# Optimization experiments

Hardware: AMD Instinct MI355X
Metric: run time of the kernel (lower is better)

The kernel has to match this reference:

```python
import jax, jax.numpy as jnp
import numpy as np

D = 768


def _rope(x):
    # interleaved RoPE over the FULL hidden dim (applied before head split, as in source)
    S, d = x.shape[-2], x.shape[-1]
    pos = jnp.arange(S, dtype=x.dtype)[:, None]                      # [S,1]
    theta = jnp.power(jnp.asarray(10000.0, x.dtype),
                      -2.0 * jnp.arange(d // 2, dtype=x.dtype) / d)  # [d/2]
    ang = pos * theta                                                # [S,d/2]
    cos2 = jnp.repeat(jnp.cos(ang), 2, axis=-1)                      # [S,d]
    sin2 = jnp.repeat(jnp.sin(ang), 2, axis=-1)
    x2 = jnp.stack([-x[..., 1::2], x[..., ::2]], axis=-1).reshape(x.shape)
    return x * cos2 + x2 * sin2


def _attn(q_in, kv_in, wq, bq, wk, bk, wv, bv, n_heads):
    # shared core of SelfAttention (n_heads=1) and MultiheadAttention (n_heads=8)
    B, Sq, Dm = q_in.shape
    Sk = kv_in.shape[1]
    Q = _rope(q_in @ wq + bq)
    K = _rope(kv_in @ wk + bk)
    V = kv_in @ wv + bv
    hd = Dm // n_heads
    Q = Q.reshape(B, Sq, n_heads, hd).transpose(0, 2, 1, 3)
    K = K.reshape(B, Sk, n_heads, hd).transpose(0, 2, 1, 3)
    V = V.reshape(B, Sk, n_heads, hd).transpose(0, 2, 1, 3)
    scores = jnp.einsum('bhqd,bhkd->bhqk', Q, K) * 8.0  # source multiplies by 8, no 1/sqrt(d)
    p = jax.nn.softmax(scores, axis=-1)
    out = jnp.einsum('bhqk,bhkd->bhqd', p, V)
    return out.transpose(0, 2, 1, 3).reshape(B, Sq, Dm)


def _ffn(x, w1, b1, w2, b2):
    return jax.nn.silu(x @ w1 + b1) @ w2 + b2


def _gate(x):
    # F = F * softmax(F, -1) + F
    return x * jax.nn.softmax(x, axis=-1) + x


def setup_inputs() -> dict:
    key = jax.random.key(0)
    ks = jax.random.split(key, 32)
    B, S, L = 32, 512, 100
    s = 1.0 / np.sqrt(D)

    def lin(k):
        kw, kb = jax.random.split(k)
        return (jax.random.normal(kw, (D, D), jnp.float32) * s,
                jax.random.normal(kb, (D,), jnp.float32) * 0.01)

    inp = {}
    inp['text_embedding'] = jax.random.normal(ks[0], (B, S, D), jnp.float32)
    inp['visual_ids'] = jax.random.randint(ks[1], (B, S), 0, L)
    inp['acoustic_ids'] = jax.random.randint(ks[2], (B, S), 0, L)
    # embedding tables (label_size+1 rows, last row is padding_idx -> zeros)
    vt = jax.random.normal(ks[3], (L + 1, D), jnp.float32)
    at = jax.random.normal(ks[4], (L + 1, D), jnp.float32)
    inp['vis_table'] = vt.at[L].set(0.0)
    inp['ac_table'] = at.at[L].set(0.0)
    (inp['hv_wq'], inp['hv_bq']) = lin(ks[5])
    (inp['hv_wk'], inp['hv_bk']) = lin(ks[6])
    (inp['hv_wv'], inp['hv_bv']) = lin(ks[7])
    (inp['ha_wq'], inp['ha_bq']) = lin(ks[8])
    (inp['ha_wk'], inp['ha_bk']) = lin(ks[9])
    (inp['ha_wv'], inp['ha_bv']) = lin(ks[10])
    (inp['ht_wq'], inp['ht_bq']) = lin(ks[11])
    (inp['ht_wk'], inp['ht_bk']) = lin(ks[12])
    (inp['ht_wv'], inp['ht_bv']) = lin(ks[13])
    (inp['ht_fcw'], inp['ht_fcb']) = lin(ks[14])
    (inp['ffn_w1'], inp['ffn_b1']) = lin(ks[15])
    (inp['ffn_w2'], inp['ffn_b2']) = lin(ks[16])
    kw, kb = jax.random.split(ks[17])
    inp['cat_w'] = jax.random.normal(kw, (2 * D, D), jnp.float32) * (1.0 / np.sqrt(2 * D))
    inp['cat_b'] = jax.random.normal(kb, (D,), jnp.float32) * 0.01
    return inp


def reference(text_embedding, vis_table, ac_table,
              hv_wq, hv_bq, hv_wk, hv_bk, hv_wv, hv_bv,
              ha_wq, ha_bq, ha_wk, ha_bk, ha_wv, ha_bv,
              ht_wq, ht_bq, ht_wk, ht_bk, ht_wv, ht_bv, ht_fcw, ht_fcb,
              ffn_w1, ffn_b1, ffn_w2, ffn_b2, cat_w, cat_b,
              visual_ids, acoustic_ids):
    hv = lambda q, kv: _attn(q, kv, hv_wq, hv_bq, hv_wk, hv_bk, hv_wv, hv_bv, 1)
    ha = lambda q, kv: _attn(q, kv, ha_wq, ha_bq, ha_wk, ha_bk, ha_wv, ha_bv, 1)

    visual_ = vis_table[visual_ids]       # [B,S,D]
    acoustic_ = ac_table[acoustic_ids]

    visual_ = hv(text_embedding, visual_)
    acoustic_ = ha(text_embedding, acoustic_)

    F1 = jnp.concatenate([visual_, acoustic_], axis=-1) @ cat_w + cat_b
    F1 = _ffn(_gate(F1), ffn_w1, ffn_b1, ffn_w2, ffn_b2)

    v = hv(visual_, acoustic_)
    a = ha(acoustic_, visual_)
    F2 = jnp.concatenate([v, a], axis=-1) @ cat_w + cat_b
    F2 = _ffn(_gate(F2), ffn_w1, ffn_b1, ffn_w2, ffn_b2)

    F3 = _attn(F1, text_embedding, ht_wq, ht_bq, ht_wk, ht_bk, ht_wv, ht_bv, 8)
    F3 = F3 @ ht_fcw + ht_fcb
    F3 = _ffn(_gate(F3), ffn_w1, ffn_b1, ffn_w2, ffn_b2)

    es = text_embedding + F1 + F2 + F3
    return _gate(es)
```

## Files before the change

kernel.cpp:

```cpp
#include <hip/hip_runtime.h>
#include <stdint.h>
#include <math.h>


typedef unsigned short USH;
typedef __attribute__((ext_vector_type(8))) short short8;
typedef __attribute__((ext_vector_type(4))) float floatx4;

#define MFMA16(a, b, c) __builtin_amdgcn_mfma_f32_16x16x32_bf16((a), (b), (c), 0, 0, 0)

static constexpr int NB = 32;
static constexpr int SS = 512;
static constexpr int DD = 768;
static constexpr int MM = NB * SS;

__device__ __forceinline__ float bf2f(USH h) {
    return __uint_as_float(((unsigned)h) << 16);
}
__device__ __forceinline__ USH f2bf(float x) {
    unsigned u = __float_as_uint(x);
    return (USH)((u + 0x7fffu + ((u >> 16) & 1u)) >> 16);
}
__device__ __forceinline__ void split3(float x, USH &h, USH &m, USH &l) {
    h = f2bf(x);
    const float r1 = x - bf2f(h);
    m = f2bf(r1);
    const float r2 = r1 - bf2f(m);
    l = f2bf(r2);
}
__device__ __forceinline__ void split3x8(const float* v, short8 &H, short8 &M, short8 &L) {
#pragma unroll
    for (int j = 0; j < 8; ++j) {
        USH h, m, l;
        split3(v[j], h, m, l);
        H[j] = (short)h; M[j] = (short)m; L[j] = (short)l;
    }
}
__device__ __forceinline__ uint2 pk4(USH a, USH b, USH c, USH d) {
    uint2 r;
    r.x = (unsigned)a | ((unsigned)b << 16);
    r.y = (unsigned)c | ((unsigned)d << 16);
    return r;
}

struct TransArgs {
    const float* in[13];
    USH* o0[13]; USH* o1[13]; USH* o2[13];
    int R[13];
};

__global__ __launch_bounds__(256) void trans_k(TransArgs a) {
    const int mi = blockIdx.z;
    const float* __restrict__ in = a.in[mi];
    USH* __restrict__ o0 = a.o0[mi];
    USH* __restrict__ o1 = a.o1[mi];
    USH* __restrict__ o2 = a.o2[mi];
    const int R = a.R[mi];
    const int bx = blockIdx.x, by = blockIdx.y;
    if (bx * 32 >= R) return;
    __shared__ float t[32][33];
    const int tx = threadIdx.x & 31, ty = threadIdx.x >> 5;
#pragma unroll
    for (int i = 0; i < 4; ++i)
        t[ty + i * 8][tx] = in[(size_t)(bx * 32 + ty + i * 8) * 768 + by * 32 + tx];
    __syncthreads();
#pragma unroll
    for (int i = 0; i < 4; ++i) {
        USH h, m, l;
        split3(t[tx][ty + i * 8], h, m, l);
        const size_t o = (size_t)(by * 32 + ty + i * 8) * R + bx * 32 + tx;
        o0[o] = h; o1[o] = m; o2[o] = l;
    }
}

__global__ __launch_bounds__(256) void gather_k(const int* __restrict__ ids,
                                                const float* __restrict__ table,
                                                float* __restrict__ dst) {
    const int g  = blockIdx.x * 256 + threadIdx.x;
    const int m  = g / 192;
    const int c4 = (g - m * 192) * 4;
    const int id = ids[m];
    *(float4*)(dst + (size_t)m * DD + c4) =
        *(const float4*)(table + (size_t)id * DD + c4);
}

__global__ __launch_bounds__(256) void gemm_k(
    const float* __restrict__ A0, const float* __restrict__ A1,
    const USH* __restrict__ B0, const USH* __restrict__ B1, const USH* __restrict__ B2,
    int ldb, const float* __restrict__ bias,
    float* __restrict__ C, USH* __restrict__ S0p, USH* __restrict__ S1p,
    USH* __restrict__ S2p, int K, int act, int tout, int Mc)
{
    __shared__ __align__(16) USH sA0[4096], sA1[4096], sA2[4096];
    __shared__ __align__(16) USH sB0[4096], sB1[4096], sB2[4096];

    const int tid  = threadIdx.x;
    const int lane = tid & 63;
    const int w    = tid >> 6;
    const int quad = lane >> 4, l15 = lane & 15;
    const int wm = (w >> 1) * 64, wn = (w & 1) * 64;
    const int gm0 = blockIdx.x * 128, gn0 = blockIdx.y * 128;

    const int i0 = tid * 2, i1 = tid * 2 + 1;
    const int r0 = i0 >> 2, c0 = (i0 & 3) << 3;
    const int r1 = i1 >> 2, c1 = (i1 & 3) << 3;

    const floatx4 zero = {0.f, 0.f, 0.f, 0.f};
    floatx4 acc[4][4];
#pragma unroll
    for (int i = 0; i < 4; ++i)
#pragma unroll
        for (int j = 0; j < 4; ++j) acc[i][j] = zero;

    for (int k0 = 0; k0 < K; k0 += 32) {
        const float* __restrict__ A = (k0 < 768) ? A0 : A1;
        const int kof = (k0 < 768) ? k0 : (k0 - 768);

        *(uint4*)&sB0[r0 * 32 + c0] = *(const uint4*)(B0 + (size_t)(gn0 + r0) * ldb + k0 + c0);
        *(uint4*)&sB0[r1 * 32 + c1] = *(const uint4*)(B0 + (size_t)(gn0 + r1) * ldb + k0 + c1);
        *(uint4*)&sB1[r0 * 32 + c0] = *(const uint4*)(B1 + (size_t)(gn0 + r0) * ldb + k0 + c0);
        *(uint4*)&sB1[r1 * 32 + c1] = *(const uint4*)(B1 + (size_t)(gn0 + r1) * ldb + k0 + c1);
        *(uint4*)&sB2[r0 * 32 + c0] = *(const uint4*)(B2 + (size_t)(gn0 + r0) * ldb + k0 + c0);
        *(uint4*)&sB2[r1 * 32 + c1] = *(const uint4*)(B2 + (size_t)(gn0 + r1) * ldb + k0 + c1);

#pragma unroll
        for (int u = 0; u < 4; ++u) {
            const int idx = tid + u * 256;
            const int r = idx >> 3, c = (idx & 7) * 4;
            const float4 v = *(const float4*)(A + (size_t)(gm0 + r) * 768 + kof + c);
            USH h[4], m[4], l[4];
            split3(v.x, h[0], m[0], l[0]);
            split3(v.y, h[1], m[1], l[1]);
            split3(v.z, h[2], m[2], l[2]);
            split3(v.w, h[3], m[3], l[3]);
            *(uint2*)&sA0[r * 32 + c] = pk4(h[0], h[1], h[2], h[3]);
            *(uint2*)&sA1[r * 32 + c] = pk4(m[0], m[1], m[2], m[3]);
            *(uint2*)&sA2[r * 32 + c] = pk4(l[0], l[1], l[2], l[3]);
        }
        __syncthreads();

        short8 a0[4], a1f[4], a2[4], b0[4], b1f[4], b2[4];
#pragma unroll
        for (int t = 0; t < 4; ++t) {
            const int ao = (wm + t * 16 + l15) * 32 + quad * 8;
            const int bo = (wn + t * 16 + l15) * 32 + quad * 8;
            a0[t]  = *(const short8*)&sA0[ao];
            a1f[t] = *(const short8*)&sA1[ao];
            a2[t]  = *(const short8*)&sA2[ao];
            b0[t]  = *(const short8*)&sB0[bo];
            b1f[t] = *(const short8*)&sB1[bo];
            b2[t]  = *(const short8*)&sB2[bo];
        }
#pragma unroll
        for (int i = 0; i < 4; ++i)
#pragma unroll
            for (int j = 0; j < 4; ++j) acc[i][j] = MFMA16(a0[i],  b0[j],  acc[i][j]);
#pragma unroll
        for (int i = 0; i < 4; ++i)
#pragma unroll
            for (int j = 0; j < 4; ++j) acc[i][j] = MFMA16(a0[i],  b1f[j], acc[i][j]);
#pragma unroll
        for (int i = 0; i < 4; ++i)
#pragma unroll
            for (int j = 0; j < 4; ++j) acc[i][j] = MFMA16(a1f[i], b0[j],  acc[i][j]);
#pragma unroll
        for (int i = 0; i < 4; ++i)
#pragma unroll
            for (int j = 0; j < 4; ++j) acc[i][j] = MFMA16(a0[i],  b2[j],  acc[i][j]);
#pragma unroll
        for (int i = 0; i < 4; ++i)
#pragma unroll
            for (int j = 0; j < 4; ++j) acc[i][j] = MFMA16(a2[i],  b0[j],  acc[i][j]);
#pragma unroll
        for (int i = 0; i < 4; ++i)
#pragma unroll
            for (int j = 0; j < 4; ++j) acc[i][j] = MFMA16(a1f[i], b1f[j], acc[i][j]);
        __syncthreads();
    }

#pragma unroll
    for (int j = 0; j < 4; ++j) {
        const int col = gn0 + wn + j * 16 + l15;
        const float bv = bias[col];
#pragma unroll
        for (int i = 0; i < 4; ++i) {
#pragma unroll
            for (int r = 0; r < 4; ++r) {
                const int row = gm0 + wm + i * 16 + quad * 4 + r;
                float x = acc[i][j][r] + bv;
                if (act == 1) {
                    const float s = 1.0f / (1.0f + expf(-x));
                    x = x * s;
                }
                if (tout == 1) {
                    USH hh, mm2, ll;
                    split3(x, hh, mm2, ll);
                    const size_t o = (size_t)col * Mc + row;
                    S0p[o] = hh; S1p[o] = mm2; S2p[o] = ll;
                } else if (tout == 2) {
                    C[(size_t)col * Mc + row] = x;
                } else {
                    C[(size_t)row * 768 + col] = x;
                }
            }
        }
    }
}

__global__ __launch_bounds__(256) void tab_k(float* __restrict__ tab) {
    const int p = blockIdx.x * 256 + threadIdx.x;
    const int s = p / 384;
    const int i = p - s * 384;
    const float ef = (-2.0f * (float)i) / 768.0f;
    const float th = (float)pow(10000.0, (double)ef);
    const float ang = (float)s * th;
    float sn, cs;
    sincosf(ang, &sn, &cs);
    tab[2 * p]     = cs;
    tab[2 * p + 1] = sn;
}

__global__ __launch_bounds__(256) void rope_k(float* __restrict__ X) {
    const int p = blockIdx.x * 256 + threadIdx.x;
    const int m = p / 384;
    const int i = p - m * 384;
    const int s = m & (SS - 1);
    const float ef = (-2.0f * (float)i) / 768.0f;
    const float th = (float)pow(10000.0, (double)ef);
    const float ang = (float)s * th;
    float sn, cs;
    sincosf(ang, &sn, &cs);
    float2 x = *(float2*)(X + (size_t)m * DD + 2 * i);
    float2 y;
    y.x = x.x * cs - x.y * sn;
    y.y = x.y * cs + x.x * sn;
    *(float2*)(X + (size_t)m * DD + 2 * i) = y;
}

__global__ __launch_bounds__(256) void rope_tab_k(float* __restrict__ X,
                                                  const float* __restrict__ tab) {
    const int p = blockIdx.x * 256 + threadIdx.x;
    const int m = p / 384;
    const int i = p - m * 384;
    const int s = m & (SS - 1);
    const float2 t = *(const float2*)(tab + 2 * (s * 384 + i));
    float2 x = *(float2*)(X + (size_t)m * DD + 2 * i);
    float2 y;
    y.x = x.x * t.x - x.y * t.y;
    y.y = x.y * t.x + x.x * t.y;
    *(float2*)(X + (size_t)m * DD + 2 * i) = y;
}

__global__ __launch_bounds__(256) void rope_split_tab_k(
    const float* __restrict__ X, const float* __restrict__ tab,
    USH* __restrict__ P0, USH* __restrict__ P1, USH* __restrict__ P2)
{
    const int p = blockIdx.x * 256 + threadIdx.x;
    const int m = p / 384;
    const int i = p - m * 384;
    const int s = m & (SS - 1);
    const float2 t = *(const float2*)(tab + 2 * (s * 384 + i));
    const float2 x = *(const float2*)(X + (size_t)m * DD + 2 * i);
    float2 y;
    y.x = x.x * t.x - x.y * t.y;
    y.y = x.y * t.x + x.x * t.y;
    USH h0, m0, l0, h1, m1, l1;
    split3(y.x, h0, m0, l0);
    split3(y.y, h1, m1, l1);
    const size_t o = (size_t)m * DD + 2 * i;
    *(unsigned*)&P0[o] = (unsigned)h0 | ((unsigned)h1 << 16);
    *(unsigned*)&P1[o] = (unsigned)m0 | ((unsigned)m1 << 16);
    *(unsigned*)&P2[o] = (unsigned)l0 | ((unsigned)l1 << 16);
}

__global__ __launch_bounds__(256) void attn_fast_k(
    const float* __restrict__ Q,
    const USH* __restrict__ KH, const USH* __restrict__ KM, const USH* __restrict__ KL,
    const USH* __restrict__ VH, const USH* __restrict__ VM, const USH* __restrict__ VL,
    float* __restrict__ O, int H, int hd, int Mc)
{
    __shared__ __align__(16) float S[16][520];
    __shared__ __align__(16) USH P2buf[16 * 520];
    __shared__ float red[16][16];
    __shared__ float stat[16];

    const int tid  = threadIdx.x;
    const int lane = tid & 63;
    const int w    = tid >> 6;
    const int quad = lane >> 4, l15 = lane & 15;
    const int b = blockIdx.y / H;
    const int h = blockIdx.y - b * H;
    const int q0 = blockIdx.x * 16;

    const floatx4 zero = {0.f, 0.f, 0.f, 0.f};

    floatx4 acc[8];
#pragma unroll
    for (int t = 0; t < 8; ++t) acc[t] = zero;

    const size_t qbase  = ((size_t)(b * SS + q0 + l15)) * DD + h * hd;
    const size_t kstrip = ((size_t)(b * SS + w * 128 + l15)) * DD + h * hd;
    const int nks = hd >> 5;
    for (int ks = 0; ks < nks; ++ks) {
        const int co = ks * 32 + quad * 8;
        float qv[8];
        *(float4*)&qv[0] = *(const float4*)(Q + qbase + co);
        *(float4*)&qv[4] = *(const float4*)(Q + qbase + co + 4);
        short8 qh, qm, ql;
        split3x8(qv, qh, qm, ql);

        size_t ka = kstrip + co;
        short8 khc = *(const short8*)&KH[ka];
        short8 kmc = *(const short8*)&KM[ka];
        short8 klc = *(const short8*)&KL[ka];
#pragma unroll
        for (int t = 0; t < 8; ++t) {
            short8 khn = khc, kmn = kmc, kln = klc;
            if (t < 7) {
                const size_t kb = ka + (size_t)(t + 1) * 16 * DD;
                khn = *(const short8*)&KH[kb];
                kmn = *(const short8*)&KM[kb];
                kln = *(const short8*)&KL[kb];
            }
            acc[t] = MFMA16(qh, khc, acc[t]);
            acc[t] = MFMA16(qh, kmc, acc[t]);
            acc[t] = MFMA16(qm, khc, acc[t]);
            acc[t] = MFMA16(qh, klc, acc[t]);
            acc[t] = MFMA16(ql, khc, acc[t]);
            acc[t] = MFMA16(qm, kmc, acc[t]);
            __builtin_amdgcn_sched_barrier(0);
            khc = khn; kmc = kmn; klc = kln;
        }
    }
#pragma unroll
    for (int t = 0; t < 8; ++t)
#pragma unroll
        for (int r = 0; r < 4; ++r)
            S[quad * 4 + r][w * 128 + t * 16 + l15] = acc[t][r] * 8.0f;
    __syncthreads();

    const int row = tid >> 4, c16 = tid & 15;
    const int cb = c16 * 32;
    float mx = -3.4e38f;
#pragma unroll 8
    for (int c = 0; c < 32; ++c) mx = fmaxf(mx, S[row][cb + c]);
    red[row][c16] = mx;
    __syncthreads();
    if (c16 == 0) {
        float m2 = red[row][0];
#pragma unroll
        for (int j = 1; j < 16; ++j) m2 = fmaxf(m2, red[row][j]);
        stat[row] = m2;
    }
    __syncthreads();
    mx = stat[row];
    float ev[32];
    float sum = 0.f;
#pragma unroll 8
    for (int c = 0; c < 32; ++c) {
        ev[c] = expf(S[row][cb + c] - mx);
        sum += ev[c];
    }
    red[row][c16] = sum;
    __syncthreads();
    if (c16 == 0) {
        float s2 = 0.f;
#pragma unroll
        for (int j = 0; j < 16; ++j) s2 += red[row][j];
        stat[row] = s2;
    }
    __syncthreads();
    const float den = stat[row];
    USH* const P0 = (USH*)&S[0][0];
    USH* const P1 = P0 + 16 * 520;
    USH* const P2 = P2buf;
#pragma unroll 8
    for (int c = 0; c < 32; ++c) {
        const float pr = ev[c] / den;
        USH hh, mm, ll;
        split3(pr, hh, mm, ll);
        P0[row * 520 + cb + c] = hh;
        P1[row * 520 + cb + c] = mm;
        P2[row * 520 + cb + c] = ll;
    }
    __syncthreads();

    const int nnt = hd >> 4;
    for (int nt = w; nt < nnt; nt += 4) {
        floatx4 o = zero;
        const int colg = h * hd + nt * 16 + l15;
        const size_t vb = (size_t)colg * Mc + b * SS;
#pragma unroll 2
        for (int ks = 0; ks < 16; ++ks) {
            const int ko = ks * 32 + quad * 8;
            const short8 ph = *(const short8*)&P0[l15 * 520 + ko];
            const short8 pm = *(const short8*)&P1[l15 * 520 + ko];
            const short8 pl = *(const short8*)&P2[l15 * 520 + ko];
            const short8 vh = *(const short8*)&VH[vb + ko];
            const short8 vm = *(const short8*)&VM[vb + ko];
            const short8 vl = *(const short8*)&VL[vb + ko];
            o = MFMA16(ph, vh, o);
            o = MFMA16(ph, vm, o);
            o = MFMA16(pm, vh, o);
            o = MFMA16(ph, vl, o);
            o = MFMA16(pl, vh, o);
            o = MFMA16(pm, vm, o);
        }
#pragma unroll
        for (int r = 0; r < 4; ++r) {
            const int orow = b * SS + q0 + quad * 4 + r;
            O[(size_t)orow * 768 + colg] = o[r];
        }
    }
}

__global__ __launch_bounds__(256) void attn_k(
    const float* __restrict__ Q, const float* __restrict__ Kp,
    const float* __restrict__ Vt, float* __restrict__ O,
    int H, int hd, int Mc)
{
    __shared__ __align__(16) float S[16][520];
    __shared__ __align__(16) USH P2buf[16 * 520];
    __shared__ float red[16][16];
    __shared__ float stat[16];

    const int tid  = threadIdx.x;
    const int lane = tid & 63;
    const int w    = tid >> 6;
    const int quad = lane >> 4, l15 = lane & 15;
    const int b = blockIdx.y / H;
    const int h = blockIdx.y - b * H;
    const int q0 = blockIdx.x * 16;

    const floatx4 zero = {0.f, 0.f, 0.f, 0.f};

    floatx4 acc[8];
#pragma unroll
    for (int t = 0; t < 8; ++t) acc[t] = zero;

    const size_t qbase = ((size_t)(b * SS + q0 + l15)) * DD + h * hd;
    const int nks = hd >> 5;
    for (int ks = 0; ks < nks; ++ks) {
        const int co = ks * 32 + quad * 8;
        float qv[8];
        *(float4*)&qv[0] = *(const float4*)(Q + qbase + co);
        *(float4*)&qv[4] = *(const float4*)(Q + qbase + co + 4);
        short8 qh, qm, ql;
        split3x8(qv, qh, qm, ql);
#pragma unroll
        for (int t = 0; t < 8; ++t) {
            const size_t kb = ((size_t)(b * SS + w * 128 + t * 16 + l15)) * DD + h * hd + co;
            float kv[8];
            *(float4*)&kv[0] = *(const float4*)(Kp + kb);
            *(float4*)&kv[4] = *(const float4*)(Kp + kb + 4);
            short8 kh, km, kl;
            split3x8(kv, kh, km, kl);
            acc[t] = MFMA16(qh, kh, acc[t]);
            acc[t] = MFMA16(qh, km, acc[t]);
            acc[t] = MFMA16(qm, kh, acc[t]);
            acc[t] = MFMA16(qh, kl, acc[t]);
            acc[t] = MFMA16(ql, kh, acc[t]);
            acc[t] = MFMA16(qm, km, acc[t]);
        }
    }
#pragma unroll
    for (int t = 0; t < 8; ++t)
#pragma unroll
        for (int r = 0; r < 4; ++r)
            S[quad * 4 + r][w * 128 + t * 16 + l15] = acc[t][r] * 8.0f;
    __syncthreads();

    const int row = tid >> 4, c16 = tid & 15;
    const int cb = c16 * 32;
    float mx = -3.4e38f;
#pragma unroll 8
    for (int c = 0; c < 32; ++c) mx = fmaxf(mx, S[row][cb + c]);
    red[row][c16] = mx;
    __syncthreads();
    if (c16 == 0) {
        float m2 = red[row][0];
#pragma unroll
        for (int j = 1; j < 16; ++j) m2 = fmaxf(m2, red[row][j]);
        stat[row] = m2;
    }
    __syncthreads();
    mx = stat[row];
    float ev[32];
    float sum = 0.f;
#pragma unroll 8
    for (int c = 0; c < 32; ++c) {
        ev[c] = expf(S[row][cb + c] - mx);
        sum += ev[c];
    }
    red[row][c16] = sum;
    __syncthreads();
    if (c16 == 0) {
        float s2 = 0.f;
#pragma unroll
        for (int j = 0; j < 16; ++j) s2 += red[row][j];
        stat[row] = s2;
    }
    __syncthreads();
    const float den = stat[row];
    USH* const P0 = (USH*)&S[0][0];
    USH* const P1 = P0 + 16 * 520;
    USH* const P2 = P2buf;
#pragma unroll 8
    for (int c = 0; c < 32; ++c) {
        const float pr = ev[c] / den;
        USH hh, mm, ll;
        split3(pr, hh, mm, ll);
        P0[row * 520 + cb + c] = hh;
        P1[row * 520 + cb + c] = mm;
        P2[row * 520 + cb + c] = ll;
    }
    __syncthreads();

    const int nnt = hd >> 4;
    for (int nt = w; nt < nnt; nt += 4) {
        floatx4 o = zero;
        const int colg = h * hd + nt * 16 + l15;
        const size_t vb = (size_t)colg * Mc + b * SS;
        for (int ks = 0; ks < 16; ++ks) {
            const int ko = ks * 32 + quad * 8;
            const short8 ph = *(const short8*)&P0[l15 * 520 + ko];
            const short8 pm = *(const short8*)&P1[l15 * 520 + ko];
            const short8 pl = *(const short8*)&P2[l15 * 520 + ko];
            float vv[8];
            *(float4*)&vv[0] = *(const float4*)(Vt + vb + ko);
            *(float4*)&vv[4] = *(const float4*)(Vt + vb + ko + 4);
            short8 vh, vm, vl;
            split3x8(vv, vh, vm, vl);
            o = MFMA16(ph, vh, o);
            o = MFMA16(ph, vm, o);
            o = MFMA16(pm, vh, o);
            o = MFMA16(ph, vl, o);
            o = MFMA16(pl, vh, o);
            o = MFMA16(pm, vm, o);
        }
#pragma unroll
        for (int r = 0; r < 4; ++r) {
            const int orow = b * SS + q0 + quad * 4 + r;
            O[(size_t)orow * 768 + colg] = o[r];
        }
    }
}

__global__ __launch_bounds__(256) void gate_k(float* __restrict__ X) {
    __shared__ float red[256];
    const int r = blockIdx.x, tid = threadIdx.x;
    const size_t base = (size_t)r * DD;
    float x[3];
#pragma unroll
    for (int j = 0; j < 3; ++j) x[j] = X[base + tid + j * 256];
    float mx = fmaxf(x[0], fmaxf(x[1], x[2]));
    red[tid] = mx;
    __syncthreads();
    for (int s = 128; s > 0; s >>= 1) {
        if (tid < s) red[tid] = fmaxf(red[tid], red[tid + s]);
        __syncthreads();
    }
    mx = red[0];
    __syncthreads();
    float e[3];
    float sum = 0.f;
#pragma unroll
    for (int j = 0; j < 3; ++j) { e[j] = expf(x[j] - mx); sum += e[j]; }
    red[tid] = sum;
    __syncthreads();
    for (int s = 128; s > 0; s >>= 1) {
        if (tid < s) red[tid] += red[tid + s];
        __syncthreads();
    }
    const float den = red[0];
#pragma unroll
    for (int j = 0; j < 3; ++j)
        X[base + tid + j * 256] = x[j] * (e[j] / den) + x[j];
}

__global__ __launch_bounds__(256) void final_k(
    const float* __restrict__ text,
    const float* __restrict__ F1, const float* __restrict__ F2,
    const float* __restrict__ F3, float* __restrict__ out)
{
    __shared__ float red[256];
    const int r = blockIdx.x, tid = threadIdx.x;
    const size_t base = (size_t)r * DD;
    float x[3];
#pragma unroll
    for (int j = 0; j < 3; ++j) {
        const int c = tid + j * 256;
        x[j] = ((text[base + c] + F1[base + c]) + F2[base + c]) + F3[base + c];
    }
    float mx = fmaxf(x[0], fmaxf(x[1], x[2]));
    red[tid] = mx;
    __syncthreads();
    for (int s = 128; s > 0; s >>= 1) {
        if (tid < s) red[tid] = fmaxf(red[tid], red[tid + s]);
        __syncthreads();
    }
    mx = red[0];
    __syncthreads();
    float e[3];
    float sum = 0.f;
#pragma unroll
    for (int j = 0; j < 3; ++j) { e[j] = expf(x[j] - mx); sum += e[j]; }
    red[tid] = sum;
    __syncthreads();
    for (int s = 128; s > 0; s >>= 1) {
        if (tid < s) red[tid] += red[tid + s];
        __syncthreads();
    }
    const float den = red[0];
#pragma unroll
    for (int j = 0; j < 3; ++j) {
        const int c = tid + j * 256;
        out[base + c] = x[j] * (e[j] / den) + x[j];
    }
}

extern "C" void kernel_launch(void* const* d_in, const int* in_sizes, int n_in,
                              void* d_out, int out_size, void* d_ws, size_t ws_size,
                              hipStream_t stream)
{
    (void)in_sizes; (void)n_in; (void)out_size;

    const float* text    = (const float*)d_in[0];
    const int*   vis_ids = (const int*)d_in[1];
    const int*   ac_ids  = (const int*)d_in[2];
    const float* vis_tab = (const float*)d_in[3];
    const float* ac_tab  = (const float*)d_in[4];
    const float* hv_wq = (const float*)d_in[5],  *hv_bq = (const float*)d_in[6];
    const float* hv_wk = (const float*)d_in[7],  *hv_bk = (const float*)d_in[8];
    const float* hv_wv = (const float*)d_in[9],  *hv_bv = (const float*)d_in[10];
    const float* ha_wq = (const float*)d_in[11], *ha_bq = (const float*)d_in[12];
    const float* ha_wk = (const float*)d_in[13], *ha_bk = (const float*)d_in[14];
    const float* ha_wv = (const float*)d_in[15], *ha_bv = (const float*)d_in[16];
    const float* ht_wq = (const float*)d_in[17], *ht_bq = (const float*)d_in[18];
    const float* ht_wk = (const float*)d_in[19], *ht_bk = (const float*)d_in[20];
    const float* ht_wv = (const float*)d_in[21], *ht_bv = (const float*)d_in[22];
    const float* ht_fcw = (const float*)d_in[23], *ht_fcb = (const float*)d_in[24];
    const float* ffn_w1 = (const float*)d_in[25], *ffn_b1 = (const float*)d_in[26];
    const float* ffn_w2 = (const float*)d_in[27], *ffn_b2 = (const float*)d_in[28];
    const float* cat_w  = (const float*)d_in[29], *cat_b  = (const float*)d_in[30];

    const size_t SQ   = (size_t)768 * 768;
    const size_t WUSH = 3 * (12 * SQ + (size_t)768 * 1536);
    const size_t TABF = (size_t)512 * 384 * 2;
    int Mc = 0, fast = 0;
    for (int cand = MM; cand >= 512; cand >>= 1) {
        const size_t nf = WUSH * sizeof(USH) + TABF * 4 + (size_t)cand * 768 * 28;
        const size_t ns = WUSH * sizeof(USH) + (size_t)cand * 768 * 24;
        if (nf <= ws_size) { Mc = cand; fast = 1; break; }
        if (ns <= ws_size) { Mc = cand; fast = 0; break; }
    }
    if (Mc == 0) return;
    const int nchunk = MM / Mc;
    const int chB    = Mc / SS;

    USH* p = (USH*)d_ws;
    USH *wt0[13], *wt1[13], *wt2[13];
    for (int i = 0; i < 13; ++i) {
        const size_t sz = (i == 12) ? (size_t)768 * 1536 : SQ;
        wt0[i] = p; p += sz;
        wt1[i] = p; p += sz;
        wt2[i] = p; p += sz;
    }

    TransArgs ta;
    const float* tin[13] = {hv_wq, hv_wk, hv_wv, ha_wq, ha_wk, ha_wv,
                            ht_wq, ht_wk, ht_wv, ht_fcw, ffn_w1, ffn_w2, cat_w};
    for (int i = 0; i < 13; ++i) {
        ta.in[i] = tin[i]; ta.o0[i] = wt0[i]; ta.o1[i] = wt1[i]; ta.o2[i] = wt2[i];
        ta.R[i] = (i == 12) ? 1536 : 768;
    }
    trans_k<<<dim3(48, 24, 13), 256, 0, stream>>>(ta);

    const size_t PSZ = (size_t)Mc * 768;
    const dim3 gg(Mc / 128, DD / 128), gb(256);
    const int ropeg = Mc * 384 / 256;
    const float* NULF = nullptr;
    USH* const NUSH = nullptr;

    if (fast) {
        float* tab = (float*)p;
        float* fp  = tab + TABF;
        float *A_ = fp + 0 * PSZ, *B_ = fp + 1 * PSZ;
        float *C_ = fp + 2 * PSZ, *F_ = fp + 3 * PSZ;
        USH* KH = (USH*)(fp + 4 * PSZ);
        USH* KM = KH + PSZ;  USH* KL = KM + PSZ;
        USH* VH = KL + PSZ;  USH* VM = VH + PSZ;  USH* VL = VM + PSZ;

        tab_k<<<(512 * 384) / 256, 256, 0, stream>>>(tab);

#define GEMM(A0P, A1P, WI, LDB, BIAS, CP, KK, ACT) \
    gemm_k<<<gg, gb, 0, stream>>>(A0P, A1P, wt0[WI], wt1[WI], wt2[WI], LDB, BIAS, \
                                  CP, NUSH, NUSH, NUSH, KK, ACT, 0, Mc)
#define GEMMV(A0P, WI, BIAS) \
    gemm_k<<<gg, gb, 0, stream>>>(A0P, NULF, wt0[WI], wt1[WI], wt2[WI], 768, BIAS, \
                                  (float*)nullptr, VH, VM, VL, 768, 0, 1, Mc)
#define ROPE(XP)  rope_tab_k<<<ropeg, 256, 0, stream>>>(XP, tab)
#define RSPL(XP)  rope_split_tab_k<<<ropeg, 256, 0, stream>>>(XP, tab, KH, KM, KL)
#define ATTNF(QP, OP, HH, HD) \
    attn_fast_k<<<dim3(SS / 16, chB * (HH)), 256, 0, stream>>>(QP, KH, KM, KL, \
                                                  VH, VM, VL, OP, HH, HD, Mc)
#define GATE(XP) gate_k<<<Mc, 256, 0, stream>>>(XP)

        for (int c = 0; c < nchunk; ++c) {
            const float* tx = text + (size_t)c * PSZ;
            const int* vi = vis_ids + (size_t)c * Mc;
            const int* ai = ac_ids  + (size_t)c * Mc;
            float* outc = (float*)d_out + (size_t)c * PSZ;

            gather_k<<<Mc * 192 / 256, 256, 0, stream>>>(vi, vis_tab, A_);
            gather_k<<<Mc * 192 / 256, 256, 0, stream>>>(ai, ac_tab, B_);

            GEMM(tx, NULF, 0, 768, hv_bq, C_, 768, 0);
            GEMM(A_, NULF, 1, 768, hv_bk, outc, 768, 0);
            GEMMV(A_, 2, hv_bv);
            ROPE(C_); RSPL(outc);
            ATTNF(C_, F_, 1, 768);

            GEMM(tx, NULF, 3, 768, ha_bq, C_, 768, 0);
            GEMM(B_, NULF, 4, 768, ha_bk, outc, 768, 0);
            GEMMV(B_, 5, ha_bv);
            ROPE(C_); RSPL(outc);
            ATTNF(C_, A_, 1, 768);

            GEMM(F_, NULF, 0, 768, hv_bq, C_, 768, 0);
            GEMM(A_, NULF, 1, 768, hv_bk, outc, 768, 0);
            GEMMV(A_, 2, hv_bv);
            ROPE(C_); RSPL(outc);
            ATTNF(C_, C_, 1, 768);

            GEMM(A_, NULF, 3, 768, ha_bq, B_, 768, 0);
            GEMM(F_, NULF, 4, 768, ha_bk, outc, 768, 0);
            GEMMV(F_, 5, ha_bv);
            ROPE(B_); RSPL(outc);
            ATTNF(B_, B_, 1, 768);

            GEMM(F_, A_, 12, 1536, cat_b, outc, 1536, 0);
            GATE(outc);
            GEMM(outc, NULF, 10, 768, ffn_b1, F_, 768, 1);
            GEMM(F_, NULF, 11, 768, ffn_b2, A_, 768, 0);

            GEMM(C_, B_, 12, 1536, cat_b, outc, 1536, 0);
            GATE(outc);
            GEMM(outc, NULF, 10, 768, ffn_b1, F_, 768, 1);
            GEMM(F_, NULF, 11, 768, ffn_b2, C_, 768, 0);

            GEMM(A_, NULF, 6, 768, ht_bq, B_, 768, 0);
            GEMM(tx, NULF, 7, 768, ht_bk, outc, 768, 0);
            GEMMV(tx, 8, ht_bv);
            ROPE(B_); RSPL(outc);
            ATTNF(B_, B_, 8, 96);
            GEMM(B_, NULF, 9, 768, ht_fcb, F_, 768, 0);
            GATE(F_);
            GEMM(F_, NULF, 10, 768, ffn_b1, B_, 768, 1);
            GEMM(B_, NULF, 11, 768, ffn_b2, F_, 768, 0);

            final_k<<<Mc, 256, 0, stream>>>(tx, A_, C_, F_, outc);
        }
#undef GEMM
#undef GEMMV
#undef ROPE
#undef RSPL
#undef ATTNF
#undef GATE
    } else {
        float* fp = (float*)p;
        float *A_ = fp + 0 * PSZ, *B_ = fp + 1 * PSZ, *C_ = fp + 2 * PSZ;
        float *D_ = fp + 3 * PSZ, *E_ = fp + 4 * PSZ, *F_ = fp + 5 * PSZ;

#define GEMM(A0P, A1P, WI, LDB, BIAS, CP, KK, ACT, TOUT) \
    gemm_k<<<gg, gb, 0, stream>>>(A0P, A1P, wt0[WI], wt1[WI], wt2[WI], LDB, BIAS, \
                                  CP, NUSH, NUSH, NUSH, KK, ACT, TOUT, Mc)
#define ROPE(XP) rope_k<<<ropeg, 256, 0, stream>>>(XP)
#define ATTN(QP, KP, VP, OP, HH, HD) \
    attn_k<<<dim3(SS / 16, chB * (HH)), 256, 0, stream>>>(QP, KP, VP, OP, HH, HD, Mc)
#define GATE(XP) gate_k<<<Mc, 256, 0, stream>>>(XP)

        for (int c = 0; c < nchunk; ++c) {
            const float* tx = text + (size_t)c * PSZ;
            const int* vi = vis_ids + (size_t)c * Mc;
            const int* ai = ac_ids  + (size_t)c * Mc;
            float* outc = (float*)d_out + (size_t)c * PSZ;

            gather_k<<<Mc * 192 / 256, 256, 0, stream>>>(vi, vis_tab, A_);
            gather_k<<<Mc * 192 / 256, 256, 0, stream>>>(ai, ac_tab, B_);

            GEMM(tx, NULF, 0, 768, hv_bq, C_, 768, 0, 0);
            GEMM(A_, NULF, 1, 768, hv_bk, D_, 768, 0, 0);
            GEMM(A_, NULF, 2, 768, hv_bv, E_, 768, 0, 2);
            ROPE(C_); ROPE(D_);
            ATTN(C_, D_, E_, F_, 1, 768);

            GEMM(tx, NULF, 3, 768, ha_bq, C_, 768, 0, 0);
            GEMM(B_, NULF, 4, 768, ha_bk, D_, 768, 0, 0);
            GEMM(B_, NULF, 5, 768, ha_bv, E_, 768, 0, 2);
            ROPE(C_); ROPE(D_);
            ATTN(C_, D_, E_, A_, 1, 768);

            GEMM(F_, NULF, 0, 768, hv_bq, C_, 768, 0, 0);
            GEMM(A_, NULF, 1, 768, hv_bk, D_, 768, 0, 0);
            GEMM(A_, NULF, 2, 768, hv_bv, E_, 768, 0, 2);
            ROPE(C_); ROPE(D_);
            ATTN(C_, D_, E_, C_, 1, 768);

            GEMM(A_, NULF, 3, 768, ha_bq, B_, 768, 0, 0);
            GEMM(F_, NULF, 4, 768, ha_bk, D_, 768, 0, 0);
            GEMM(F_, NULF, 5, 768, ha_bv, E_, 768, 0, 2);
            ROPE(B_); ROPE(D_);
            ATTN(B_, D_, E_, B_, 1, 768);

            GEMM(F_, A_, 12, 1536, cat_b, D_, 1536, 0, 0);
            GATE(D_);
            GEMM(D_, NULF, 10, 768, ffn_b1, E_, 768, 1, 0);
            GEMM(E_, NULF, 11, 768, ffn_b2, F_, 768, 0, 0);

            GEMM(C_, B_, 12, 1536, cat_b, A_, 1536, 0, 0);
            GATE(A_);
            GEMM(A_, NULF, 10, 768, ffn_b1, C_, 768, 1, 0);
            GEMM(C_, NULF, 11, 768, ffn_b2, B_, 768, 0, 0);

            GEMM(F_, NULF, 6, 768, ht_bq, C_, 768, 0, 0);
            GEMM(tx, NULF, 7, 768, ht_bk, D_, 768, 0, 0);
            GEMM(tx, NULF, 8, 768, ht_bv, E_, 768, 0, 2);
            ROPE(C_); ROPE(D_);
            ATTN(C_, D_, E_, C_, 8, 96);
            GEMM(C_, NULF, 9, 768, ht_fcb, A_, 768, 0, 0);
            GATE(A_);
            GEMM(A_, NULF, 10, 768, ffn_b1, C_, 768, 1, 0);
            GEMM(C_, NULF, 11, 768, ffn_b2, D_, 768, 0, 0);

            final_k<<<Mc, 256, 0, stream>>>(tx, F_, B_, D_, outc);
        }
#undef GEMM
#undef ROPE
#undef ATTN
#undef GATE
    }
}
```

Measured before the change: 7.340 ms.

## Pre-split GEMM activations into bf16x3 planes and pipeline attention K/V loads

Activations are now split once into three bf16 planes (hi/mid/lo) by dedicated split, gather-split and gate-split kernels. A new LDS-free GEMM kernel with a 128x96 tile reads those planes directly, instead of re-splitting fp32 inputs inside every tiled GEMM. The fast attention kernel now register-prefetches all eight K and V fragments one step ahead and swizzles the block order. This removes repeated per-GEMM conversion work and improves latency hiding, at the cost of extra split launches, more register pressure, and GEMM operands read straight from global memory without shared-memory reuse.

```diff
diff --git a/kernel.cpp b/kernel.cpp
--- a/kernel.cpp
+++ b/kernel.cpp
@@ -73,6 +73,37 @@
     }
 }
 
+__global__ __launch_bounds__(256) void split_k(const float* __restrict__ X,
+        USH* __restrict__ P0, USH* __restrict__ P1, USH* __restrict__ P2) {
+    const size_t g = (size_t)blockIdx.x * 256 + threadIdx.x;
+    float v[8];
+    *(float4*)&v[0] = ((const float4*)X)[2 * g];
+    *(float4*)&v[4] = ((const float4*)X)[2 * g + 1];
+    short8 H8, M8, L8;
+    split3x8(v, H8, M8, L8);
+    ((short8*)P0)[g] = H8;
+    ((short8*)P1)[g] = M8;
+    ((short8*)P2)[g] = L8;
+}
+
+__global__ __launch_bounds__(256) void gather_split_k(const int* __restrict__ ids,
+        const float* __restrict__ table,
+        USH* __restrict__ P0, USH* __restrict__ P1, USH* __restrict__ P2) {
+    const int g = blockIdx.x * 256 + threadIdx.x;
+    const int m = g / 96;
+    const int e = (g - m * 96) * 8;
+    const int id = ids[m];
+    float v[8];
+    *(float4*)&v[0] = *(const float4*)(table + (size_t)id * DD + e);
+    *(float4*)&v[4] = *(const float4*)(table + (size_t)id * DD + e + 4);
+    short8 H8, M8, L8;
+    split3x8(v, H8, M8, L8);
+    const size_t o = (size_t)m * DD + e;
+    *(short8*)&P0[o] = H8;
+    *(short8*)&P1[o] = M8;
+    *(short8*)&P2[o] = L8;
+}
+
 __global__ __launch_bounds__(256) void gather_k(const int* __restrict__ ids,
                                                 const float* __restrict__ table,
                                                 float* __restrict__ dst) {
@@ -84,12 +115,101 @@
         *(const float4*)(table + (size_t)id * DD + c4);
 }
 
+__global__ __launch_bounds__(256) void gemm_ps_k(
+    const USH* __restrict__ AH0, const USH* __restrict__ AM0, const USH* __restrict__ AL0,
+    const USH* __restrict__ AH1, const USH* __restrict__ AM1, const USH* __restrict__ AL1,
+    const USH* __restrict__ B0, const USH* __restrict__ B1, const USH* __restrict__ B2,
+    int ldb, const float* __restrict__ bias,
+    float* __restrict__ C, USH* __restrict__ S0p, USH* __restrict__ S1p,
+    USH* __restrict__ S2p, int K, int act, int tout, int Mc)
+{
+    const int tid  = threadIdx.x;
+    const int lane = tid & 63;
+    const int w    = tid >> 6;
+    const int quad = lane >> 4, l15 = lane & 15;
+    const int wm = (w >> 1) * 64, wn = (w & 1) * 48;
+    const int gm0 = blockIdx.x * 128, gn0 = blockIdx.y * 96;
+
+    const floatx4 zero = {0.f, 0.f, 0.f, 0.f};
+    floatx4 acc[4][3];
+#pragma unroll
+    for (int i = 0; i < 4; ++i)
+#pragma unroll
+        for (int j = 0; j < 3; ++j) acc[i][j] = zero;
+
+    const size_t abase = (size_t)(gm0 + wm + l15) * 768 + quad * 8;
+    const size_t bbase = (size_t)(gn0 + wn + l15) * ldb + quad * 8;
+
+#pragma unroll 2
+    for (int k0 = 0; k0 < K; k0 += 32) {
+        const USH* __restrict__ AH = (k0 < 768) ? AH0 : AH1;
+        const USH* __restrict__ AM = (k0 < 768) ? AM0 : AM1;
+        const USH* __restrict__ AL = (k0 < 768) ? AL0 : AL1;
+        const int kof = (k0 < 768) ? k0 : (k0 - 768);
+
+        short8 a0[4], a1f[4], a2[4];
+#pragma unroll
+        for (int t = 0; t < 4; ++t) {
+            const size_t ao = abase + (size_t)t * (16 * 768) + kof;
+            a0[t]  = *(const short8*)&AH[ao];
+            a1f[t] = *(const short8*)&AM[ao];
+            a2[t]  = *(const short8*)&AL[ao];
+        }
+#pragma unroll
+        for (int j = 0; j < 3; ++j) {
+            const size_t bo = bbase + (size_t)j * 16 * ldb + k0;
+            const short8 b0  = *(const short8*)&B0[bo];
+            const short8 b1f = *(const short8*)&B1[bo];
+            const short8 b2  = *(const short8*)&B2[bo];
+#pragma unroll
+            for (int i = 0; i < 4; ++i) {
+                acc[i][j] = MFMA16(a0[i],  b0,  acc[i][j]);
+                acc[i][j] = MFMA16(a0[i],  b1f, acc[i][j]);
+                acc[i][j] = MFMA16(a1f[i], b0,  acc[i][j]);
+                acc[i][j] = MFMA16(a0[i],  b2,  acc[i][j]);
+                acc[i][j] = MFMA16(a2[i],  b0,  acc[i][j]);
+                acc[i][j] = MFMA16(a1f[i], b1f, acc[i][j]);
+            }
+        }
+    }
+
+#pragma unroll
+    for (int j = 0; j < 3; ++j) {
+        const int col = gn0 + wn + j * 16 + l15;
+        const float bv = bias[col];
+#pragma unroll
+        for (int i = 0; i < 4; ++i) {
+#pragma unroll
+            for (int r = 0; r < 4; ++r) {
+                const int row = gm0 + wm + i * 16 + quad * 4 + r;
+                float x = acc[i][j][r] + bv;
+                if (act == 1) {
+                    const float s = 1.0f / (1.0f + expf(-x));
+                    x = x * s;
+                }
+                if (tout == 1) {
+                    USH hh, mm2, ll;
+                    split3(x, hh, mm2, ll);
+                    const size_t o = (size_t)col * Mc + row;
+                    S0p[o] = hh; S1p[o] = mm2; S2p[o] = ll;
+                } else if (tout == 3) {
+                    USH hh, mm2, ll;
+                    split3(x, hh, mm2, ll);
+                    const size_t o = (size_t)row * 768 + col;
+                    S0p[o] = hh; S1p[o] = mm2; S2p[o] = ll;
+                } else {
+                    C[(size_t)row * 768 + col] = x;
+                }
+            }
+        }
+    }
+}
+
 __global__ __launch_bounds__(256) void gemm_k(
     const float* __restrict__ A0, const float* __restrict__ A1,
     const USH* __restrict__ B0, const USH* __restrict__ B1, const USH* __restrict__ B2,
     int ldb, const float* __restrict__ bias,
-    float* __restrict__ C, USH* __restrict__ S0p, USH* __restrict__ S1p,
-    USH* __restrict__ S2p, int K, int act, int tout, int Mc)
+    float* __restrict__ C, int K, int act, int tout, int Mc)
 {
     __shared__ __align__(16) USH sA0[4096], sA1[4096], sA2[4096];
     __shared__ __align__(16) USH sB0[4096], sB1[4096], sB2[4096];
@@ -192,16 +312,9 @@
                     const float s = 1.0f / (1.0f + expf(-x));
                     x = x * s;
                 }
-                if (tout == 1) {
-                    USH hh, mm2, ll;
-                    split3(x, hh, mm2, ll);
-                    const size_t o = (size_t)col * Mc + row;
-                    S0p[o] = hh; S1p[o] = mm2; S2p[o] = ll;
-                } else if (tout == 2) {
-                    C[(size_t)col * Mc + row] = x;
-                } else {
-                    C[(size_t)row * 768 + col] = x;
-                }
+                const size_t o = (tout == 2) ? ((size_t)col * Mc + row)
+                                             : ((size_t)row * 768 + col);
+                C[o] = x;
             }
         }
     }
@@ -288,9 +401,15 @@
     const int lane = tid & 63;
     const int w    = tid >> 6;
     const int quad = lane >> 4, l15 = lane & 15;
-    const int b = blockIdx.y / H;
-    const int h = blockIdx.y - b * H;
-    const int q0 = blockIdx.x * 16;
+
+    const int nbx = gridDim.x;
+    const int tot = nbx * gridDim.y;
+    int bid = blockIdx.y * nbx + blockIdx.x;
+    bid = (bid & 7) * (tot >> 3) + (bid >> 3);
+    const int yy = bid / nbx;
+    const int q0 = (bid - yy * nbx) * 16;
+    const int b = yy / H;
+    const int h = yy - b * H;
 
     const floatx4 zero = {0.f, 0.f, 0.f, 0.f};
 
@@ -298,40 +417,55 @@
 #pragma unroll
     for (int t = 0; t < 8; ++t) acc[t] = zero;
 
-    const size_t qbase  = ((size_t)(b * SS + q0 + l15)) * DD + h * hd;
-    const size_t kstrip = ((size_t)(b * SS + w * 128 + l15)) * DD + h * hd;
+    const size_t qbase  = ((size_t)(b * SS + q0 + l15)) * DD + h * hd + quad * 8;
+    const size_t kstrip = ((size_t)(b * SS + w * 128 + l15)) * DD + h * hd + quad * 8;
     const int nks = hd >> 5;
+    const size_t TOFF = (size_t)16 * DD;
+
+    short8 k0h,k0m,k0l, k1h,k1m,k1l, k2h,k2m,k2l, k3h,k3m,k3l,
+           k4h,k4m,k4l, k5h,k5m,k5l, k6h,k6m,k6l, k7h,k7m,k7l;
+#define KLD(D, OFS) { const size_t _o = (OFS); \
+        k##D##h = *(const short8*)&KH[_o]; \
+        k##D##m = *(const short8*)&KM[_o]; \
+        k##D##l = *(const short8*)&KL[_o]; }
+
+    KLD(0, kstrip + 0 * TOFF)
+    KLD(1, kstrip + 1 * TOFF)
+    KLD(2, kstrip + 2 * TOFF)
+    KLD(3, kstrip + 3 * TOFF)
+    KLD(4, kstrip + 4 * TOFF)
+    KLD(5, kstrip + 5 * TOFF)
+    KLD(6, kstrip + 6 * TOFF)
+    KLD(7, kstrip + 7 * TOFF)
+
+    float qv[8];
+    *(float4*)&qv[0] = *(const float4*)(Q + qbase);
+    *(float4*)&qv[4] = *(const float4*)(Q + qbase + 4);
+    short8 qh, qm, ql;
+    split3x8(qv, qh, qm, ql);
+
+#define ST1(T) \
+        acc[T] = MFMA16(qh, k##T##h, acc[T]); \
+        acc[T] = MFMA16(qh, k##T##m, acc[T]); \
+        acc[T] = MFMA16(qm, k##T##h, acc[T]); \
+        acc[T] = MFMA16(qh, k##T##l, acc[T]); \
+        acc[T] = MFMA16(ql, k##T##h, acc[T]); \
+        acc[T] = MFMA16(qm, k##T##m, acc[T]); \
+        KLD(T, knxt + T * TOFF) \
+        __builtin_amdgcn_sched_barrier(0);
+
     for (int ks = 0; ks < nks; ++ks) {
-        const int co = ks * 32 + quad * 8;
-        float qv[8];
-        *(float4*)&qv[0] = *(const float4*)(Q + qbase + co);
-        *(float4*)&qv[4] = *(const float4*)(Q + qbase + co + 4);
-        short8 qh, qm, ql;
-        split3x8(qv, qh, qm, ql);
-
-        size_t ka = kstrip + co;
-        short8 khc = *(const short8*)&KH[ka];
-        short8 kmc = *(const short8*)&KM[ka];
-        short8 klc = *(const short8*)&KL[ka];
-#pragma unroll
-        for (int t = 0; t < 8; ++t) {
-            short8 khn = khc, kmn = kmc, kln = klc;
-            if (t < 7) {
-                const size_t kb = ka + (size_t)(t + 1) * 16 * DD;
-                khn = *(const short8*)&KH[kb];
-                kmn = *(const short8*)&KM[kb];
-                kln = *(const short8*)&KL[kb];
-            }
-            acc[t] = MFMA16(qh, khc, acc[t]);
-            acc[t] = MFMA16(qh, kmc, acc[t]);
-            acc[t] = MFMA16(qm, khc, acc[t]);
-            acc[t] = MFMA16(qh, klc, acc[t]);
-            acc[t] = MFMA16(ql, khc, acc[t]);
-            acc[t] = MFMA16(qm, kmc, acc[t]);
-            __builtin_amdgcn_sched_barrier(0);
-            khc = khn; kmc = kmn; klc = kln;
-        }
-    }
+        const int nx = (ks + 1 < nks) ? (ks + 1) : ks;
+        const size_t knxt = kstrip + (size_t)nx * 32;
+        float qn[8];
+        *(float4*)&qn[0] = *(const float4*)(Q + qbase + (size_t)nx * 32);
+        *(float4*)&qn[4] = *(const float4*)(Q + qbase + (size_t)nx * 32 + 4);
+        ST1(0) ST1(1) ST1(2) ST1(3) ST1(4) ST1(5) ST1(6) ST1(7)
+        split3x8(qn, qh, qm, ql);
+    }
+#undef ST1
+#undef KLD
+
 #pragma unroll
     for (int t = 0; t < 8; ++t)
 #pragma unroll
@@ -386,32 +520,56 @@
     __syncthreads();
 
     const int nnt = hd >> 4;
+    const int pb = l15 * 520 + quad * 8;
+
+    short8 v0h,v0m,v0l, v1h,v1m,v1l, v2h,v2m,v2l, v3h,v3m,v3l,
+           v4h,v4m,v4l, v5h,v5m,v5l, v6h,v6m,v6l, v7h,v7m,v7l;
+#define VLD(D, OFS) { const size_t _o = (OFS); \
+        v##D##h = *(const short8*)&VH[_o]; \
+        v##D##m = *(const short8*)&VM[_o]; \
+        v##D##l = *(const short8*)&VL[_o]; }
+#define ST3(KS, D) { \
+        const short8 ph = *(const short8*)&P0[pb + (KS) * 32]; \
+        const short8 pm = *(const short8*)&P1[pb + (KS) * 32]; \
+        const short8 pl = *(const short8*)&P2[pb + (KS) * 32]; \
+        o = MFMA16(ph, v##D##h, o); \
+        o = MFMA16(ph, v##D##m, o); \
+        o = MFMA16(pm, v##D##h, o); \
+        o = MFMA16(ph, v##D##l, o); \
+        o = MFMA16(pl, v##D##h, o); \
+        o = MFMA16(pm, v##D##m, o); \
+        VLD(D, ((KS) < 8) ? (vb + ((KS) + 8) * 32) : (vb2 + ((KS) - 8) * 32)) \
+        __builtin_amdgcn_sched_barrier(0); }
+
+    {
+        const int colg0 = h * hd + w * 16 + l15;
+        const size_t vbp = (size_t)colg0 * Mc + b * SS + quad * 8;
+        VLD(0, vbp + 0 * 32)
+        VLD(1, vbp + 1 * 32)
+        VLD(2, vbp + 2 * 32)
+        VLD(3, vbp + 3 * 32)
+        VLD(4, vbp + 4 * 32)
+        VLD(5, vbp + 5 * 32)
+        VLD(6, vbp + 6 * 32)
+        VLD(7, vbp + 7 * 32)
+    }
     for (int nt = w; nt < nnt; nt += 4) {
+        const int colg = h * hd + nt * 16 + l15;
+        const size_t vb  = (size_t)colg * Mc + b * SS + quad * 8;
+        const size_t vb2 = (nt + 4 < nnt) ? (vb + (size_t)64 * Mc) : vb;
         floatx4 o = zero;
-        const int colg = h * hd + nt * 16 + l15;
-        const size_t vb = (size_t)colg * Mc + b * SS;
-#pragma unroll 2
-        for (int ks = 0; ks < 16; ++ks) {
-            const int ko = ks * 32 + quad * 8;
-            const short8 ph = *(const short8*)&P0[l15 * 520 + ko];
-            const short8 pm = *(const short8*)&P1[l15 * 520 + ko];
-            const short8 pl = *(const short8*)&P2[l15 * 520 + ko];
-            const short8 vh = *(const short8*)&VH[vb + ko];
-            const short8 vm = *(const short8*)&VM[vb + ko];
-            const short8 vl = *(const short8*)&VL[vb + ko];
-            o = MFMA16(ph, vh, o);
-            o = MFMA16(ph, vm, o);
-            o = MFMA16(pm, vh, o);
-            o = MFMA16(ph, vl, o);
-            o = MFMA16(pl, vh, o);
-            o = MFMA16(pm, vm, o);
-        }
+        ST3(0, 0)  ST3(1, 1)  ST3(2, 2)  ST3(3, 3)
+        ST3(4, 4)  ST3(5, 5)  ST3(6, 6)  ST3(7, 7)
+        ST3(8, 0)  ST3(9, 1)  ST3(10, 2) ST3(11, 3)
+        ST3(12, 4) ST3(13, 5) ST3(14, 6) ST3(15, 7)
 #pragma unroll
         for (int r = 0; r < 4; ++r) {
             const int orow = b * SS + q0 + quad * 4 + r;
             O[(size_t)orow * 768 + colg] = o[r];
         }
     }
+#undef ST3
+#undef VLD
 }
 
 __global__ __launch_bounds__(256) void attn_k(
@@ -578,6 +736,45 @@
         X[base + tid + j * 256] = x[j] * (e[j] / den) + x[j];
 }
 
+__global__ __launch_bounds__(256) void gate_split_k(float* __restrict__ X,
+        USH* __restrict__ P0, USH* __restrict__ P1, USH* __restrict__ P2) {
+    __shared__ float red[256];
+    const int r = blockIdx.x, tid = threadIdx.x;
+    const size_t base = (size_t)r * DD;
+    float x[3];
+#pragma unroll
+    for (int j = 0; j < 3; ++j) x[j] = X[base + tid + j * 256];
+    float mx = fmaxf(x[0], fmaxf(x[1], x[2]));
+    red[tid] = mx;
+    __syncthreads();
+    for (int s = 128; s > 0; s >>= 1) {
+        if (tid < s) red[tid] = fmaxf(red[tid], red[tid + s]);
+        __syncthreads();
+    }
+    mx = red[0];
+    __syncthreads();
+    float e[3];
+    float sum = 0.f;
+#pragma unroll
+    for (int j = 0; j < 3; ++j) { e[j] = expf(x[j] - mx); sum += e[j]; }
+    red[tid] = sum;
+    __syncthreads();
+    for (int s = 128; s > 0; s >>= 1) {
+        if (tid < s) red[tid] += red[tid + s];
+        __syncthreads();
+    }
+    const float den = red[0];
+#pragma unroll
+    for (int j = 0; j < 3; ++j) {
+        const int c = tid + j * 256;
+        const float y = x[j] * (e[j] / den) + x[j];
+        X[base + c] = y;
+        USH hh, mm, ll;
+        split3(y, hh, mm, ll);
+        P0[base + c] = hh; P1[base + c] = mm; P2[base + c] = ll;
+    }
+}
+
 __global__ __launch_bounds__(256) void final_k(
     const float* __restrict__ text,
     const float* __restrict__ F1, const float* __restrict__ F2,
@@ -677,8 +874,8 @@
     trans_k<<<dim3(48, 24, 13), 256, 0, stream>>>(ta);
 
     const size_t PSZ = (size_t)Mc * 768;
-    const dim3 gg(Mc / 128, DD / 128), gb(256);
     const int ropeg = Mc * 384 / 256;
+    const dim3 gb(256);
     const float* NULF = nullptr;
     USH* const NUSH = nullptr;
 
@@ -693,18 +890,28 @@
 
         tab_k<<<(512 * 384) / 256, 256, 0, stream>>>(tab);
 
-#define GEMM(A0P, A1P, WI, LDB, BIAS, CP, KK, ACT) \
-    gemm_k<<<gg, gb, 0, stream>>>(A0P, A1P, wt0[WI], wt1[WI], wt2[WI], LDB, BIAS, \
-                                  CP, NUSH, NUSH, NUSH, KK, ACT, 0, Mc)
-#define GEMMV(A0P, WI, BIAS) \
-    gemm_k<<<gg, gb, 0, stream>>>(A0P, NULF, wt0[WI], wt1[WI], wt2[WI], 768, BIAS, \
-                                  (float*)nullptr, VH, VM, VL, 768, 0, 1, Mc)
+        const dim3 gg2(Mc / 128, 8);
+        const int splg = Mc * 3 / 8;
+
+#define SPL(XP)   split_k<<<splg, 256, 0, stream>>>(XP, KH, KM, KL)
+#define SPLV(XP)  split_k<<<splg, 256, 0, stream>>>(XP, VH, VM, VL)
+#define GTH(IDS, TB) gather_split_k<<<splg, 256, 0, stream>>>(IDS, TB, KH, KM, KL)
+#define GEMMK(WI, BIAS, CP) gemm_ps_k<<<gg2, gb, 0, stream>>>(KH, KM, KL, KH, KM, KL, \
+        wt0[WI], wt1[WI], wt2[WI], 768, BIAS, CP, NUSH, NUSH, NUSH, 768, 0, 0, Mc)
+#define GEMMKV(WI, BIAS) gemm_ps_k<<<gg2, gb, 0, stream>>>(KH, KM, KL, KH, KM, KL, \
+        wt0[WI], wt1[WI], wt2[WI], 768, BIAS, (float*)nullptr, VH, VM, VL, 768, 0, 1, Mc)
+#define GEMMKH() gemm_ps_k<<<gg2, gb, 0, stream>>>(KH, KM, KL, KH, KM, KL, \
+        wt0[10], wt1[10], wt2[10], 768, ffn_b1, (float*)nullptr, VH, VM, VL, 768, 1, 3, Mc)
+#define GEMMVO(WI, BIAS, CP) gemm_ps_k<<<gg2, gb, 0, stream>>>(VH, VM, VL, VH, VM, VL, \
+        wt0[WI], wt1[WI], wt2[WI], 768, BIAS, CP, NUSH, NUSH, NUSH, 768, 0, 0, Mc)
+#define GEMMCAT(CP) gemm_ps_k<<<gg2, gb, 0, stream>>>(KH, KM, KL, VH, VM, VL, \
+        wt0[12], wt1[12], wt2[12], 1536, cat_b, CP, NUSH, NUSH, NUSH, 1536, 0, 0, Mc)
+#define GATES(XP) gate_split_k<<<Mc, 256, 0, stream>>>(XP, KH, KM, KL)
 #define ROPE(XP)  rope_tab_k<<<ropeg, 256, 0, stream>>>(XP, tab)
 #define RSPL(XP)  rope_split_tab_k<<<ropeg, 256, 0, stream>>>(XP, tab, KH, KM, KL)
 #define ATTNF(QP, OP, HH, HD) \
     attn_fast_k<<<dim3(SS / 16, chB * (HH)), 256, 0, stream>>>(QP, KH, KM, KL, \
                                                   VH, VM, VL, OP, HH, HD, Mc)
-#define GATE(XP) gate_k<<<Mc, 256, 0, stream>>>(XP)
 
         for (int c = 0; c < nchunk; ++c) {
             const float* tx = text + (size_t)c * PSZ;
@@ -712,69 +919,74 @@
             const int* ai = ac_ids  + (size_t)c * Mc;
             float* outc = (float*)d_out + (size_t)c * PSZ;
 
-            gather_k<<<Mc * 192 / 256, 256, 0, stream>>>(vi, vis_tab, A_);
-            gather_k<<<Mc * 192 / 256, 256, 0, stream>>>(ai, ac_tab, B_);
-
-            GEMM(tx, NULF, 0, 768, hv_bq, C_, 768, 0);
-            GEMM(A_, NULF, 1, 768, hv_bk, outc, 768, 0);
-            GEMMV(A_, 2, hv_bv);
+            SPL(tx);  GEMMK(0, hv_bq, C_);
+            GTH(vi, vis_tab);
+            GEMMK(1, hv_bk, outc);
+            GEMMKV(2, hv_bv);
             ROPE(C_); RSPL(outc);
             ATTNF(C_, F_, 1, 768);
 
-            GEMM(tx, NULF, 3, 768, ha_bq, C_, 768, 0);
-            GEMM(B_, NULF, 4, 768, ha_bk, outc, 768, 0);
-            GEMMV(B_, 5, ha_bv);
+            SPL(tx);  GEMMK(3, ha_bq, C_);
+            GTH(ai, ac_tab);
+            GEMMK(4, ha_bk, outc);  GEMMKV(5, ha_bv);
             ROPE(C_); RSPL(outc);
             ATTNF(C_, A_, 1, 768);
 
-            GEMM(F_, NULF, 0, 768, hv_bq, C_, 768, 0);
-            GEMM(A_, NULF, 1, 768, hv_bk, outc, 768, 0);
-            GEMMV(A_, 2, hv_bv);
+            SPL(F_);  GEMMK(0, hv_bq, C_);
+            SPL(A_);  GEMMK(1, hv_bk, outc);  GEMMKV(2, hv_bv);
             ROPE(C_); RSPL(outc);
             ATTNF(C_, C_, 1, 768);
 
-            GEMM(A_, NULF, 3, 768, ha_bq, B_, 768, 0);
-            GEMM(F_, NULF, 4, 768, ha_bk, outc, 768, 0);
-            GEMMV(F_, 5, ha_bv);
+            SPL(A_);  GEMMK(3, ha_bq, B_);
+            SPL(F_);  GEMMK(4, ha_bk, outc);  GEMMKV(5, ha_bv);
             ROPE(B_); RSPL(outc);
             ATTNF(B_, B_, 1, 768);
 
-            GEMM(F_, A_, 12, 1536, cat_b, outc, 1536, 0);
-            GATE(outc);
-            GEMM(outc, NULF, 10, 768, ffn_b1, F_, 768, 1);
-            GEMM(F_, NULF, 11, 768, ffn_b2, A_, 768, 0);
-
-            GEMM(C_, B_, 12, 1536, cat_b, outc, 1536, 0);
-            GATE(outc);
-            GEMM(outc, NULF, 10, 768, ffn_b1, F_, 768, 1);
-            GEMM(F_, NULF, 11, 768, ffn_b2, C_, 768, 0);
-
-            GEMM(A_, NULF, 6, 768, ht_bq, B_, 768, 0);
-            GEMM(tx, NULF, 7, 768, ht_bk, outc, 768, 0);
-            GEMMV(tx, 8, ht_bv);
+            SPL(F_);
+            SPLV(A_);
+            GEMMCAT(outc);
+            GATES(outc);
+            GEMMKH();
+            GEMMVO(11, ffn_b2, A_);
+
+            SPL(C_);  SPLV(B_);
+            GEMMCAT(outc);
+            GATES(outc);
+            GEMMKH();
+            GEMMVO(11, ffn_b2, C_);
+
+            SPL(A_);  GEMMK(6, ht_bq, B_);
+            SPL(tx);  GEMMK(7, ht_bk, outc);  GEMMKV(8, ht_bv);
             ROPE(B_); RSPL(outc);
             ATTNF(B_, B_, 8, 96);
-            GEMM(B_, NULF, 9, 768, ht_fcb, F_, 768, 0);
-            GATE(F_);
-            GEMM(F_, NULF, 10, 768, ffn_b1, B_, 768, 1);
-            GEMM(B_, NULF, 11, 768, ffn_b2, F_, 768, 0);
+            SPL(B_);  GEMMK(9, ht_fcb, F_);
+            GATES(F_);
+            GEMMKH();
+            GEMMVO(11, ffn_b2, F_);
 
             final_k<<<Mc, 256, 0, stream>>>(tx, A_, C_, F_, outc);
         }
-#undef GEMM
-#undef GEMMV
+#undef SPL
+#undef SPLV
+#undef GTH
+#undef GEMMK
+#undef GEMMKV
+#undef GEMMKH
+#undef GEMMVO
+#undef GEMMCAT
+#undef GATES
 #undef ROPE
 #undef RSPL
 #undef ATTNF
-#undef GATE
     } else {
         float* fp = (float*)p;
         float *A_ = fp + 0 * PSZ, *B_ = fp + 1 * PSZ, *C_ = fp + 2 * PSZ;
         float *D_ = fp + 3 * PSZ, *E_ = fp + 4 * PSZ, *F_ = fp + 5 * PSZ;
+        const dim3 gg(Mc / 128, DD / 128);
 
 #define GEMM(A0P, A1P, WI, LDB, BIAS, CP, KK, ACT, TOUT) \
     gemm_k<<<gg, gb, 0, stream>>>(A0P, A1P, wt0[WI], wt1[WI], wt2[WI], LDB, BIAS, \
-                                  CP, NUSH, NUSH, NUSH, KK, ACT, TOUT, Mc)
+                                  CP, KK, ACT, TOUT, Mc)
 #define ROPE(XP) rope_k<<<ropeg, 256, 0, stream>>>(XP)
 #define ATTN(QP, KP, VP, OP, HH, HD) \
     attn_k<<<dim3(SS / 16, chB * (HH)), 256, 0, stream>>>(QP, KP, VP, OP, HH, HD, Mc)
```

Measured after the change: 10.33 ms. +40.7%, slower.
